# Performance work log

Measured on AMD Instinct MI355X. Metric: run time of the kernel, lower is better.

## Reference

```python
import jax, jax.numpy as jnp
import numpy as np

D_MODEL = 256
D_INNER = 512   # expand_factor * d_model
D_STATE = 64
DT_RANK = 4     # ceil(d_model / 64)
D_CONV = 4
B = 8
L = 144


def setup_inputs() -> dict:
    key = jax.random.key(0)
    ks = jax.random.split(key, 8)
    s = lambda k, shp, sc=0.02: jax.random.normal(k, shp, jnp.float32) * sc
    x = jax.random.normal(ks[0], (B, L, D_MODEL), jnp.float32)
    lastin = jnp.zeros((B, D_INNER, D_STATE), jnp.float32)  # accepted but unused by the scan
    W_in = s(ks[1], (2 * D_INNER, D_MODEL))              # in_proj (no bias)
    conv_w = s(ks[2], (D_INNER, 1, D_CONV), 0.1)          # depthwise conv kernel [O, I/groups, K]
    conv_b = jnp.zeros((D_INNER,), jnp.float32)
    W_x = s(ks[3], (DT_RANK + 2 * D_STATE, D_INNER))      # x_proj (no bias)
    W_dt = s(ks[4], (D_INNER, DT_RANK), 0.1)
    b_dt = jnp.full((D_INNER,), -4.0, jnp.float32)        # softplus -> small dt, like mamba init
    A_log = jnp.log(jnp.tile(jnp.arange(1, D_STATE + 1, dtype=jnp.float32), (D_INNER, 1)))
    Dp = jnp.ones((D_INNER,), jnp.float32)
    W_out = s(ks[5], (D_MODEL, D_INNER))                  # out_proj (no bias)
    return dict(x=x, lastin=lastin, W_in=W_in, conv_w=conv_w, conv_b=conv_b,
                W_x=W_x, W_dt=W_dt, b_dt=b_dt, A_log=A_log, Dp=Dp, W_out=W_out)


def _forward(x, lastin, W_in, conv_w, conv_b, W_x, W_dt, b_dt, A_log, Dp, W_out):
    # in_proj and split
    xz = jnp.einsum('bld,ed->ble', x, W_in)               # [B, L, 2*d_inner]
    ix, z = jnp.split(xz, 2, axis=-1)

    # depthwise causal-ish conv1d: torch padding=2 then slice [:L] == padding (2, 1)
    ix = jnp.swapaxes(ix, 1, 2)                            # [B, d_inner, L]
    ix = jax.lax.conv_general_dilated(
        ix, conv_w, window_strides=(1,), padding=[(2, 1)],
        feature_group_count=D_INNER, dimension_numbers=('NCH', 'OIH', 'NCH'))
    ix = ix + conv_b[None, :, None]
    ix = jnp.swapaxes(ix, 1, 2)                            # [B, L, d_inner]
    ix = jax.nn.silu(ix)

    # ssm parameterization
    A = -jnp.exp(A_log)                                    # [d_inner, d_state]
    dBC = jnp.einsum('bld,ed->ble', ix, W_x)               # [B, L, dt_rank + 2*d_state]
    dt_r = dBC[..., :DT_RANK]
    Bm = dBC[..., DT_RANK:DT_RANK + D_STATE]               # [B, L, d_state]
    Cm = dBC[..., DT_RANK + D_STATE:]                      # [B, L, d_state]
    delta = jax.nn.softplus(jnp.einsum('blr,dr->bld', dt_r, W_dt) + b_dt)  # [B, L, d_inner]

    # discretization
    deltaA = jnp.exp(delta[..., None] * A)                 # [B, L, d_inner, d_state]
    BX = (delta * ix)[..., None] * Bm[:, :, None, :]       # [B, L, d_inner, d_state]

    # sequential selective scan: h_t = deltaA_t * h_{t-1} + BX_t
    def step(h, inp):
        dA_t, bx_t = inp
        h = dA_t * h + bx_t
        return h, h

    h0 = jnp.zeros((x.shape[0], D_INNER, D_STATE), x.dtype)
    _, hs = jax.lax.scan(step, h0, (jnp.moveaxis(deltaA, 1, 0), jnp.moveaxis(BX, 1, 0)))
    # hs: [L, B, d_inner, d_state]

    y = jnp.einsum('lbdn,lbn->bld', hs, jnp.moveaxis(Cm, 1, 0))  # [B, L, d_inner]
    y = y + Dp * ix

    out = jnp.einsum('bld,ed->ble', y * jax.nn.silu(z), W_out)   # [B, L, d_model]
    return out


def reference(x, lastin, W_in, conv_w, conv_b, W_x, W_dt, b_dt, A_log, Dp, W_out):
    return _forward(x, lastin, W_in, conv_w, conv_b, W_x, W_dt, b_dt, A_log, Dp, W_out)
```

## Files before the change

kernel.cpp:

```cpp
#include <hip/hip_runtime.h>

#define B_SZ 8
#define L_SEQ 144
#define NTOK 1152
#define D_MODEL 256
#define D_INNER 512
#define D_STATE 64
#define DT_RANK 4
#define NDBC 132
#define SLAB 152064

typedef __attribute__((ext_vector_type(8))) short bf16x8;
typedef __attribute__((ext_vector_type(4))) float f32x4;

__device__ __forceinline__ void cvt8(const float4& f0, const float4& f1,
                                     int4& hi, int4& lo) {
    const float f[8] = {f0.x, f0.y, f0.z, f0.w, f1.x, f1.y, f1.z, f1.w};
    unsigned h[8], l[8];
#pragma unroll
    for (int e = 0; e < 8; ++e) {
        const unsigned u = __float_as_uint(f[e]);
        const unsigned t = u + 0x7FFFu + ((u >> 16) & 1u);
        h[e] = t >> 16;
        l[e] = __float_as_uint(f[e] - __uint_as_float(t & 0xFFFF0000u)) >> 16;
    }
    hi = make_int4((int)(h[0] | (h[1] << 16)), (int)(h[2] | (h[3] << 16)),
                   (int)(h[4] | (h[5] << 16)), (int)(h[6] | (h[7] << 16)));
    lo = make_int4((int)(l[0] | (l[1] << 16)), (int)(l[2] | (l[3] << 16)),
                   (int)(l[4] | (l[5] << 16)), (int)(l[6] | (l[7] << 16)));
}

__device__ __forceinline__ void unpack8(const int4& p0, const int4& p1,
                                        bf16x8& hv, bf16x8& lv) {
    const unsigned u[8] = {(unsigned)p0.x, (unsigned)p0.y, (unsigned)p0.z,
                           (unsigned)p0.w, (unsigned)p1.x, (unsigned)p1.y,
                           (unsigned)p1.z, (unsigned)p1.w};
    int h[4], l[4];
#pragma unroll
    for (int i = 0; i < 4; ++i) {
        h[i] = (int)((u[2 * i] >> 16) | (u[2 * i + 1] & 0xFFFF0000u));
        l[i] = (int)((u[2 * i] & 0xFFFFu) | (u[2 * i + 1] << 16));
    }
    hv = *(bf16x8*)h;
    lv = *(bf16x8*)l;
}

#define LW 40
__global__ __launch_bounds__(256) void gemm1_mfma(const float* __restrict__ W_in,
                                                  const float* __restrict__ x,
                                                  float* __restrict__ xz) {
    __shared__ unsigned short Ah[64][LW], Al[64][LW], Bh[64][LW], Bl[64][LW];
    const int tid = threadIdx.x;
    const int m0 = blockIdx.y * 64, n0 = blockIdx.x * 64;
    const int r = tid >> 2, kq = (tid & 3) * 8;
    const int w = tid >> 6, lane = tid & 63;
    const int wm = (w & 1) * 32, wn = (w >> 1) * 32;
    const int fr = lane & 15, fk = (lane >> 4) * 8;
    f32x4 acc[2][2] = {};
    float4 a0, a1, b0, b1;

    auto loadG = [&](const int k0) {
        const float* ap = W_in + (size_t)(m0 + r) * D_MODEL + k0 + kq;
        const float* bp = x    + (size_t)(n0 + r) * D_MODEL + k0 + kq;
        a0 = *(const float4*)ap; a1 = *(const float4*)(ap + 4);
        b0 = *(const float4*)bp; b1 = *(const float4*)(bp + 4);
    };

    loadG(0);
    for (int k0 = 0; k0 < D_MODEL; k0 += 32) {
        int4 hi, lo;
        __syncthreads();
        cvt8(a0, a1, hi, lo);
        *(int4*)&Ah[r][kq] = hi; *(int4*)&Al[r][kq] = lo;
        cvt8(b0, b1, hi, lo);
        *(int4*)&Bh[r][kq] = hi; *(int4*)&Bl[r][kq] = lo;
        __syncthreads();
        if (k0 + 32 < D_MODEL) loadG(k0 + 32);
        bf16x8 ah[2], al[2], bh[2], bl[2];
#pragma unroll
        for (int i = 0; i < 2; ++i) {
            ah[i] = *(const bf16x8*)&Ah[wm + 16 * i + fr][fk];
            al[i] = *(const bf16x8*)&Al[wm + 16 * i + fr][fk];
            bh[i] = *(const bf16x8*)&Bh[wn + 16 * i + fr][fk];
            bl[i] = *(const bf16x8*)&Bl[wn + 16 * i + fr][fk];
        }
#pragma unroll
        for (int i = 0; i < 2; ++i)
#pragma unroll
            for (int j = 0; j < 2; ++j) {
                acc[i][j] = __builtin_amdgcn_mfma_f32_16x16x32_bf16(ah[i], bh[j], acc[i][j], 0, 0, 0);
                acc[i][j] = __builtin_amdgcn_mfma_f32_16x16x32_bf16(ah[i], bl[j], acc[i][j], 0, 0, 0);
                acc[i][j] = __builtin_amdgcn_mfma_f32_16x16x32_bf16(al[i], bh[j], acc[i][j], 0, 0, 0);
            }
    }
    const int orow = (lane >> 4) * 4;
#pragma unroll
    for (int i = 0; i < 2; ++i)
#pragma unroll
        for (int j = 0; j < 2; ++j)
#pragma unroll
            for (int q = 0; q < 4; ++q)
                xz[(size_t)(m0 + wm + 16 * i + orow + q) * NTOK
                   + n0 + wn + 16 * j + fr] = acc[i][j][q];
}

__device__ __forceinline__ int bc_perm(const int p) {
    return (p < DT_RANK) ? p
         : (((p - DT_RANK) & 1) ? (DT_RANK + D_STATE + ((p - DT_RANK) >> 1))
                                : (DT_RANK + ((p - DT_RANK) >> 1)));
}

__global__ __launch_bounds__(256) void gemm2_mfma(const float* __restrict__ xz,
                                                  const float* __restrict__ W_x,
                                                  float* __restrict__ slab,
                                                  const float* __restrict__ cw,
                                                  const float* __restrict__ cb) {
    __shared__ unsigned short Ah[64][LW], Al[64][LW], Bh[64][LW], Bl[64][LW];
    const int tid = threadIdx.x;
    const int n0 = blockIdx.x * 64;
    const int m0 = blockIdx.y * 64;
    const int kbeg = blockIdx.z * 64;
    const int ar = tid >> 3, ac8 = (tid & 7) * 8;
    const int br = tid >> 2, bq8 = (tid & 3) * 8;
    const int brow = bc_perm(n0 + br);
    const int w = tid >> 6, lane = tid & 63;
    const int wm = (w & 1) * 32, wn = (w >> 1) * 32;
    const int fr = lane & 15, fk = (lane >> 4) * 8;
    const int t = (m0 + ac8) % L_SEQ;
    f32x4 acc[2][2] = {};
    slab += (size_t)blockIdx.z * SLAB;

#pragma unroll
    for (int ks = 0; ks < 2; ++ks) {
        const int k0 = kbeg + ks * 32;
        const int d = k0 + ar;
        const float* row = xz + (size_t)d * NTOK + m0 + ac8;
        const float4 a0 = *(const float4*)row;
        const float4 a1 = *(const float4*)(row + 4);
        const float xm2 = (t > 0) ? row[-2] : 0.f;
        const float xm1 = (t > 0) ? row[-1] : 0.f;
        const float xp8 = (t < L_SEQ - 8) ? row[8] : 0.f;
        const float4 cw4 = *(const float4*)(cw + d * 4);
        const float cbv = cb[d];
        float4 bv0 = make_float4(0.f, 0.f, 0.f, 0.f), bv1 = bv0;
        if (n0 + br < NDBC) {
            const float* bp = W_x + (size_t)brow * D_INNER + k0 + bq8;
            bv0 = *(const float4*)bp; bv1 = *(const float4*)(bp + 4);
        }
        __syncthreads();
        {
            const float in[11] = {xm2, xm1, a0.x, a0.y, a0.z, a0.w,
                                  a1.x, a1.y, a1.z, a1.w, xp8};
#pragma unroll
            for (int j = 0; j < 8; ++j) {
                float s = cbv;
                s = fmaf(cw4.x, in[j + 0], s);
                s = fmaf(cw4.y, in[j + 1], s);
                s = fmaf(cw4.z, in[j + 2], s);
                s = fmaf(cw4.w, in[j + 3], s);
                const float g = s * __builtin_amdgcn_rcpf(1.f + __expf(-s));
                const unsigned u = __float_as_uint(g);
                const unsigned tt = u + 0x7FFFu + ((u >> 16) & 1u);
                Ah[ac8 + j][ar] = (unsigned short)(tt >> 16);
                Al[ac8 + j][ar] = (unsigned short)(__float_as_uint(
                                     g - __uint_as_float(tt & 0xFFFF0000u)) >> 16);
            }
            int4 hi, lo;
            cvt8(bv0, bv1, hi, lo);
            *(int4*)&Bh[br][bq8] = hi; *(int4*)&Bl[br][bq8] = lo;
        }
        __syncthreads();
        bf16x8 ah[2], al[2], bh[2], bl[2];
#pragma unroll
        for (int i = 0; i < 2; ++i) {
            ah[i] = *(const bf16x8*)&Ah[wm + 16 * i + fr][fk];
            al[i] = *(const bf16x8*)&Al[wm + 16 * i + fr][fk];
            bh[i] = *(const bf16x8*)&Bh[wn + 16 * i + fr][fk];
            bl[i] = *(const bf16x8*)&Bl[wn + 16 * i + fr][fk];
        }
#pragma unroll
        for (int i = 0; i < 2; ++i)
#pragma unroll
            for (int j = 0; j < 2; ++j) {
                acc[i][j] = __builtin_amdgcn_mfma_f32_16x16x32_bf16(ah[i], bh[j], acc[i][j], 0, 0, 0);
                acc[i][j] = __builtin_amdgcn_mfma_f32_16x16x32_bf16(ah[i], bl[j], acc[i][j], 0, 0, 0);
                acc[i][j] = __builtin_amdgcn_mfma_f32_16x16x32_bf16(al[i], bh[j], acc[i][j], 0, 0, 0);
            }
    }
    const int orow = (lane >> 4) * 4;
#pragma unroll
    for (int i = 0; i < 2; ++i)
#pragma unroll
        for (int j = 0; j < 2; ++j) {
            const int gn = n0 + wn + 16 * j + fr;
            if (gn < NDBC)
#pragma unroll
                for (int q = 0; q < 4; ++q)
                    slab[(size_t)(m0 + wm + 16 * i + orow + q) * NDBC + gn]
                        = acc[i][j][q];
        }
}

__global__ __launch_bounds__(256) void gemm3_mfma(const unsigned* __restrict__ gpk,
                                                  const float* __restrict__ W_out,
                                                  float* __restrict__ slab) {
    const int tid = threadIdx.x;
    const int n0 = blockIdx.x * 64, m0 = blockIdx.y * 64;
    const int kbeg = blockIdx.z * 64;
    const int w = tid >> 6, lane = tid & 63;
    const int wm = (w & 1) * 32, wn = (w >> 1) * 32;
    const int fr = lane & 15, fk = (lane >> 4) * 8;
    f32x4 acc[2][2] = {};
    slab += (size_t)blockIdx.z * (NTOK * D_MODEL);
#pragma unroll
    for (int ks = 0; ks < 2; ++ks) {
        const int k0 = kbeg + ks * 32;
        bf16x8 ah[2], al[2], bh[2], bl[2];
#pragma unroll
        for (int i = 0; i < 2; ++i) {
            const unsigned* ap = gpk + (size_t)(m0 + wm + 16 * i + fr) * D_INNER + k0 + fk;
            unpack8(*(const int4*)ap, *(const int4*)(ap + 4), ah[i], al[i]);
        }
#pragma unroll
        for (int j = 0; j < 2; ++j) {
            const float* bp = W_out + (size_t)(n0 + wn + 16 * j + fr) * D_INNER + k0 + fk;
            int4 hi, lo;
            cvt8(*(const float4*)bp, *(const float4*)(bp + 4), hi, lo);
            bh[j] = *(bf16x8*)&hi;
            bl[j] = *(bf16x8*)&lo;
        }
#pragma unroll
        for (int i = 0; i < 2; ++i)
#pragma unroll
            for (int j = 0; j < 2; ++j) {
                acc[i][j] = __builtin_amdgcn_mfma_f32_16x16x32_bf16(ah[i], bh[j], acc[i][j], 0, 0, 0);
                acc[i][j] = __builtin_amdgcn_mfma_f32_16x16x32_bf16(ah[i], bl[j], acc[i][j], 0, 0, 0);
                acc[i][j] = __builtin_amdgcn_mfma_f32_16x16x32_bf16(al[i], bh[j], acc[i][j], 0, 0, 0);
            }
    }
    const int orow = (lane >> 4) * 4;
#pragma unroll
    for (int i = 0; i < 2; ++i)
#pragma unroll
        for (int j = 0; j < 2; ++j)
#pragma unroll
            for (int q = 0; q < 4; ++q)
                slab[(size_t)(m0 + wm + 16 * i + orow + q) * D_MODEL
                     + n0 + wn + 16 * j + fr] = acc[i][j][q];
}

__global__ __launch_bounds__(256) void reduce8_k(const float4* __restrict__ in,
                                                 float4* __restrict__ out,
                                                 const int n4, const int s4) {
    const int i = blockIdx.x * 256 + threadIdx.x;
    if (i >= n4) return;
    float4 a = in[i];
#pragma unroll
    for (int s = 1; s < 8; ++s) {
        const float4 b = in[i + s * s4];
        a.x += b.x; a.y += b.y; a.z += b.z; a.w += b.w;
    }
    out[i] = a;
}

__device__ __forceinline__ float bcast(const float v, const int i) {
    return __int_as_float(__builtin_amdgcn_readlane(__float_as_int(v), i));
}

template<int CNT>
__device__ __forceinline__ void scan_chunk(const float* __restrict__ dBC,
                                           const float* __restrict__ xz,
                                           unsigned* __restrict__ gpk,
                                           float (*__restrict__ Pw)[65],
                                           const int d, const int base, const int t0,
                                           const float An2, const float4 wdt,
                                           const float bdt, const float dpv,
                                           const float4 cw4, const float cbv,
                                           const int lane, float& h) {
    float delta_r = 0.f, dix_r = 0.f, dpix_r = 0.f, sz_r = 0.f;
    if (lane < CNT) {
        const int t = t0 + lane;
        const int tok = base + t;
        const float* row = xz + (size_t)d * NTOK + tok;
        float s0 = cbv;
        if (t >= 2) s0 = fmaf(cw4.x, row[-2], s0);
        if (t >= 1) s0 = fmaf(cw4.y, row[-1], s0);
        s0 = fmaf(cw4.z, row[0], s0);
        if (t < L_SEQ - 1) s0 = fmaf(cw4.w, row[1], s0);
        const float ixv = s0 * __builtin_amdgcn_rcpf(1.f + __expf(-s0));

        const float4 dt4 = *(const float4*)(dBC + (size_t)tok * NDBC);
        float s = fmaf(dt4.x, wdt.x, bdt);
        s = fmaf(dt4.y, wdt.y, s);
        s = fmaf(dt4.z, wdt.z, s);
        s = fmaf(dt4.w, wdt.w, s);
        const float delta = fmaxf(s, 0.f) + __logf(1.f + __expf(-fabsf(s)));
        const float zv = xz[(size_t)(D_INNER + d) * NTOK + tok];
        delta_r = delta;
        dix_r   = delta * ixv;
        dpix_r  = dpv * ixv;
        sz_r    = zv * __builtin_amdgcn_rcpf(1.f + __expf(-zv));
    }
#pragma unroll
    for (int i = 0; i < CNT; ++i) {
        const float2 bc = *(const float2*)(dBC + (size_t)(base + t0 + i) * NDBC
                                           + DT_RANK + 2 * lane);
        const float dlt = bcast(delta_r, i);
        const float dxv = bcast(dix_r, i);
        const float dA = __builtin_amdgcn_exp2f(dlt * An2);
        h = fmaf(dA, h, dxv * bc.x);
        Pw[i][lane] = h * bc.y;
    }
    const int tl = lane & 31, hf = lane >> 5;
    float s2 = 0.f;
    if (tl < CNT) {
#pragma unroll
        for (int j = 0; j < 32; ++j) s2 += Pw[tl][hf * 32 + j];
    }
    s2 += __shfl_xor(s2, 32, 64);
    if (hf == 0 && tl < CNT) {
        const float g = (s2 + dpix_r) * sz_r;
        const unsigned u = __float_as_uint(g);
        const unsigned t = u + 0x7FFFu + ((u >> 16) & 1u);
        const unsigned lo16 = __float_as_uint(
            g - __uint_as_float(t & 0xFFFF0000u)) >> 16;
        gpk[(size_t)(base + t0 + tl) * D_INNER + d] = (t & 0xFFFF0000u) | lo16;
    }
}

__global__ __launch_bounds__(256) void scan_k(const float* __restrict__ dBC,
                                              const float* __restrict__ xz,
                                              const float* __restrict__ W_dt,
                                              const float* __restrict__ b_dt,
                                              const float* __restrict__ A_log,
                                              const float* __restrict__ Dp,
                                              const float* __restrict__ conv_w,
                                              const float* __restrict__ conv_b,
                                              unsigned* __restrict__ gpk) {
    __shared__ float P[4][32][65];
    const int w = threadIdx.x >> 6, lane = threadIdx.x & 63;
    const int b = blockIdx.x >> 7, dg = blockIdx.x & 127;
    const int d = (dg << 2) | w;
    const int base = b * L_SEQ;
    const float An2 = -__expf(A_log[(d << 6) + lane]) * 1.44269504088896f;
    const float4 wdt = *(const float4*)(W_dt + (d << 2));
    const float bdt = b_dt[d], dpv = Dp[d];
    const float4 cw4 = *(const float4*)(conv_w + (d << 2));
    const float cbv = conv_b[d];
    float h = 0.f;
    scan_chunk<32>(dBC, xz, gpk, P[w], d, base, 0,   An2, wdt, bdt, dpv, cw4, cbv, lane, h);
    scan_chunk<32>(dBC, xz, gpk, P[w], d, base, 32,  An2, wdt, bdt, dpv, cw4, cbv, lane, h);
    scan_chunk<32>(dBC, xz, gpk, P[w], d, base, 64,  An2, wdt, bdt, dpv, cw4, cbv, lane, h);
    scan_chunk<32>(dBC, xz, gpk, P[w], d, base, 96,  An2, wdt, bdt, dpv, cw4, cbv, lane, h);
    scan_chunk<16>(dBC, xz, gpk, P[w], d, base, 128, An2, wdt, bdt, dpv, cw4, cbv, lane, h);
}

extern "C" void kernel_launch(void* const* d_in, const int* in_sizes, int n_in,
                              void* d_out, int out_size, void* d_ws, size_t ws_size,
                              hipStream_t stream) {
    const float* x      = (const float*)d_in[0];
    const float* W_in   = (const float*)d_in[2];
    const float* conv_w = (const float*)d_in[3];
    const float* conv_b = (const float*)d_in[4];
    const float* W_x    = (const float*)d_in[5];
    const float* W_dt   = (const float*)d_in[6];
    const float* b_dt   = (const float*)d_in[7];
    const float* A_log  = (const float*)d_in[8];
    const float* Dp     = (const float*)d_in[9];
    const float* W_out  = (const float*)d_in[10];
    float* out = (float*)d_out;

    float* ws  = (float*)d_ws;
    float* xz  = ws;
    float* dBC = xz + 1179648;
    float* sl3 = dBC + 152064;
    unsigned* gpk = (unsigned*)(sl3 + 8 * SLAB);
    float* sl6 = (float*)(gpk + NTOK * D_INNER);

    gemm1_mfma<<<dim3(18, 16), 256, 0, stream>>>(W_in, x, xz);
    gemm2_mfma<<<dim3(3, 18, 8), 256, 0, stream>>>(xz, W_x, sl3, conv_w, conv_b);
    reduce8_k<<<dim3(149), 256, 0, stream>>>((const float4*)sl3, (float4*)dBC,
                                             NTOK * NDBC / 4, NTOK * NDBC / 4);
    scan_k<<<dim3(B_SZ * 128), 256, 0, stream>>>(dBC, xz, W_dt, b_dt, A_log, Dp,
                                                 conv_w, conv_b, gpk);
    gemm3_mfma<<<dim3(4, 18, 8), 256, 0, stream>>>(gpk, W_out, sl6);
    reduce8_k<<<dim3(288), 256, 0, stream>>>((const float4*)sl6, (float4*)out,
                                             NTOK * D_MODEL / 4, NTOK * D_MODEL / 4);
}
```

Before: 130.5 us.

## Replace split-K slabs and reduce kernels with in-block warp split-K reduction

```diff
diff --git a/kernel.cpp b/kernel.cpp
--- a/kernel.cpp
+++ b/kernel.cpp
@@ -8,7 +8,6 @@
 #define D_STATE 64
 #define DT_RANK 4
 #define NDBC 132
-#define SLAB 152064
 
 typedef __attribute__((ext_vector_type(8))) short bf16x8;
 typedef __attribute__((ext_vector_type(4))) float f32x4;
@@ -43,6 +42,12 @@
     }
     hv = *(bf16x8*)h;
     lv = *(bf16x8*)l;
+}
+
+__device__ __forceinline__ int bc_perm(const int p) {
+    return (p < DT_RANK) ? p
+         : (((p - DT_RANK) & 1) ? (DT_RANK + D_STATE + ((p - DT_RANK) >> 1))
+                                : (DT_RANK + ((p - DT_RANK) >> 1)));
 }
 
 #define LW 40
@@ -104,135 +109,160 @@
                    + n0 + wn + 16 * j + fr] = acc[i][j][q];
 }
 
-__device__ __forceinline__ int bc_perm(const int p) {
-    return (p < DT_RANK) ? p
-         : (((p - DT_RANK) & 1) ? (DT_RANK + D_STATE + ((p - DT_RANK) >> 1))
-                                : (DT_RANK + ((p - DT_RANK) >> 1)));
-}
-
 __global__ __launch_bounds__(256) void gemm2_mfma(const float* __restrict__ xz,
                                                   const float* __restrict__ W_x,
-                                                  float* __restrict__ slab,
+                                                  float* __restrict__ dBC,
                                                   const float* __restrict__ cw,
                                                   const float* __restrict__ cb) {
-    __shared__ unsigned short Ah[64][LW], Al[64][LW], Bh[64][LW], Bl[64][LW];
+    __shared__ union {
+        unsigned short st[4][4][64][LW];
+        float red[4][4096];
+    } sm;
     const int tid = threadIdx.x;
     const int n0 = blockIdx.x * 64;
     const int m0 = blockIdx.y * 64;
-    const int kbeg = blockIdx.z * 64;
-    const int ar = tid >> 3, ac8 = (tid & 7) * 8;
-    const int br = tid >> 2, bq8 = (tid & 3) * 8;
-    const int brow = bc_perm(n0 + br);
     const int w = tid >> 6, lane = tid & 63;
-    const int wm = (w & 1) * 32, wn = (w >> 1) * 32;
+    const int kw = w * 128;
     const int fr = lane & 15, fk = (lane >> 4) * 8;
-    const int t = (m0 + ac8) % L_SEQ;
-    f32x4 acc[2][2] = {};
-    slab += (size_t)blockIdx.z * SLAB;
-
-#pragma unroll
-    for (int ks = 0; ks < 2; ++ks) {
-        const int k0 = kbeg + ks * 32;
-        const int d = k0 + ar;
-        const float* row = xz + (size_t)d * NTOK + m0 + ac8;
-        const float4 a0 = *(const float4*)row;
-        const float4 a1 = *(const float4*)(row + 4);
-        const float xm2 = (t > 0) ? row[-2] : 0.f;
-        const float xm1 = (t > 0) ? row[-1] : 0.f;
-        const float xp8 = (t < L_SEQ - 8) ? row[8] : 0.f;
-        const float4 cw4 = *(const float4*)(cw + d * 4);
-        const float cbv = cb[d];
-        float4 bv0 = make_float4(0.f, 0.f, 0.f, 0.f), bv1 = bv0;
-        if (n0 + br < NDBC) {
-            const float* bp = W_x + (size_t)brow * D_INNER + k0 + bq8;
-            bv0 = *(const float4*)bp; bv1 = *(const float4*)(bp + 4);
-        }
-        __syncthreads();
-        {
-            const float in[11] = {xm2, xm1, a0.x, a0.y, a0.z, a0.w,
-                                  a1.x, a1.y, a1.z, a1.w, xp8};
+    f32x4 acc[4][4] = {};
+
+    float apre[4][11];
+    float4 cwp[4];
+    float cbp[4];
+
+    auto loadA = [&](const int k0) {
+#pragma unroll
+        for (int jj = 0; jj < 4; ++jj) {
+            const int id = jj * 64 + lane;
+            const int dl = id >> 3, oct = id & 7;
+            const int d = k0 + dl;
+            const float* row = xz + (size_t)d * NTOK + m0 + oct * 8;
+            const int t = (m0 + oct * 8) % L_SEQ;
+            apre[jj][0] = (t > 0) ? row[-2] : 0.f;
+            apre[jj][1] = (t > 0) ? row[-1] : 0.f;
+            const float4 r0 = *(const float4*)row;
+            const float4 r1 = *(const float4*)(row + 4);
+            apre[jj][2] = r0.x; apre[jj][3] = r0.y; apre[jj][4] = r0.z; apre[jj][5] = r0.w;
+            apre[jj][6] = r1.x; apre[jj][7] = r1.y; apre[jj][8] = r1.z; apre[jj][9] = r1.w;
+            apre[jj][10] = (t < L_SEQ - 8) ? row[8] : 0.f;
+            cwp[jj] = *(const float4*)(cw + d * 4);
+            cbp[jj] = cb[d];
+        }
+    };
+
+    loadA(kw);
+#pragma unroll
+    for (int m = 0; m < 4; ++m) {
+        const int k0 = kw + m * 32;
+#pragma unroll
+        for (int jj = 0; jj < 4; ++jj) {
+            const int id = jj * 64 + lane;
+            const int dl = id >> 3, oct = id & 7;
 #pragma unroll
             for (int j = 0; j < 8; ++j) {
-                float s = cbv;
-                s = fmaf(cw4.x, in[j + 0], s);
-                s = fmaf(cw4.y, in[j + 1], s);
-                s = fmaf(cw4.z, in[j + 2], s);
-                s = fmaf(cw4.w, in[j + 3], s);
+                float s = cbp[jj];
+                s = fmaf(cwp[jj].x, apre[jj][j + 0], s);
+                s = fmaf(cwp[jj].y, apre[jj][j + 1], s);
+                s = fmaf(cwp[jj].z, apre[jj][j + 2], s);
+                s = fmaf(cwp[jj].w, apre[jj][j + 3], s);
                 const float g = s * __builtin_amdgcn_rcpf(1.f + __expf(-s));
                 const unsigned u = __float_as_uint(g);
                 const unsigned tt = u + 0x7FFFu + ((u >> 16) & 1u);
-                Ah[ac8 + j][ar] = (unsigned short)(tt >> 16);
-                Al[ac8 + j][ar] = (unsigned short)(__float_as_uint(
-                                     g - __uint_as_float(tt & 0xFFFF0000u)) >> 16);
+                sm.st[w][0][oct * 8 + j][dl] = (unsigned short)(tt >> 16);
+                sm.st[w][1][oct * 8 + j][dl] = (unsigned short)(__float_as_uint(
+                    g - __uint_as_float(tt & 0xFFFF0000u)) >> 16);
+            }
+        }
+#pragma unroll
+        for (int jj = 0; jj < 4; ++jj) {
+            const int id = jj * 64 + lane;
+            const int e = id >> 2, ko = (id & 3) * 8;
+            float4 b0 = make_float4(0.f, 0.f, 0.f, 0.f), b1 = b0;
+            if (n0 + e < NDBC) {
+                const float* bp = W_x + (size_t)bc_perm(n0 + e) * D_INNER + k0 + ko;
+                b0 = *(const float4*)bp; b1 = *(const float4*)(bp + 4);
             }
             int4 hi, lo;
-            cvt8(bv0, bv1, hi, lo);
-            *(int4*)&Bh[br][bq8] = hi; *(int4*)&Bl[br][bq8] = lo;
-        }
-        __syncthreads();
-        bf16x8 ah[2], al[2], bh[2], bl[2];
-#pragma unroll
-        for (int i = 0; i < 2; ++i) {
-            ah[i] = *(const bf16x8*)&Ah[wm + 16 * i + fr][fk];
-            al[i] = *(const bf16x8*)&Al[wm + 16 * i + fr][fk];
-            bh[i] = *(const bf16x8*)&Bh[wn + 16 * i + fr][fk];
-            bl[i] = *(const bf16x8*)&Bl[wn + 16 * i + fr][fk];
-        }
-#pragma unroll
-        for (int i = 0; i < 2; ++i)
-#pragma unroll
-            for (int j = 0; j < 2; ++j) {
+            cvt8(b0, b1, hi, lo);
+            *(int4*)&sm.st[w][2][e][ko] = hi;
+            *(int4*)&sm.st[w][3][e][ko] = lo;
+        }
+        if (m < 3) loadA(k0 + 32);
+        bf16x8 ah[4], al[4], bh[4], bl[4];
+#pragma unroll
+        for (int i = 0; i < 4; ++i) {
+            ah[i] = *(const bf16x8*)&sm.st[w][0][16 * i + fr][fk];
+            al[i] = *(const bf16x8*)&sm.st[w][1][16 * i + fr][fk];
+            bh[i] = *(const bf16x8*)&sm.st[w][2][16 * i + fr][fk];
+            bl[i] = *(const bf16x8*)&sm.st[w][3][16 * i + fr][fk];
+        }
+#pragma unroll
+        for (int i = 0; i < 4; ++i)
+#pragma unroll
+            for (int j = 0; j < 4; ++j) {
                 acc[i][j] = __builtin_amdgcn_mfma_f32_16x16x32_bf16(ah[i], bh[j], acc[i][j], 0, 0, 0);
                 acc[i][j] = __builtin_amdgcn_mfma_f32_16x16x32_bf16(ah[i], bl[j], acc[i][j], 0, 0, 0);
                 acc[i][j] = __builtin_amdgcn_mfma_f32_16x16x32_bf16(al[i], bh[j], acc[i][j], 0, 0, 0);
             }
     }
+    __syncthreads();
     const int orow = (lane >> 4) * 4;
 #pragma unroll
-    for (int i = 0; i < 2; ++i)
-#pragma unroll
-        for (int j = 0; j < 2; ++j) {
-            const int gn = n0 + wn + 16 * j + fr;
-            if (gn < NDBC)
-#pragma unroll
-                for (int q = 0; q < 4; ++q)
-                    slab[(size_t)(m0 + wm + 16 * i + orow + q) * NDBC + gn]
-                        = acc[i][j][q];
-        }
+    for (int i = 0; i < 4; ++i)
+#pragma unroll
+        for (int j = 0; j < 4; ++j)
+#pragma unroll
+            for (int q = 0; q < 4; ++q)
+                sm.red[w][(16 * i + orow + q) * 64 + 16 * j + fr] = acc[i][j][q];
+    __syncthreads();
+#pragma unroll
+    for (int rep = 0; rep < 4; ++rep) {
+        const int idx4 = rep * 256 + tid;
+        const int row = idx4 >> 4, col = (idx4 & 15) * 4;
+        const int gn = n0 + col;
+        if (gn < NDBC) {
+            const float4 s0 = *(const float4*)&sm.red[0][row * 64 + col];
+            const float4 s1 = *(const float4*)&sm.red[1][row * 64 + col];
+            const float4 s2 = *(const float4*)&sm.red[2][row * 64 + col];
+            const float4 s3 = *(const float4*)&sm.red[3][row * 64 + col];
+            *(float4*)(dBC + (size_t)(m0 + row) * NDBC + gn) = make_float4(
+                s0.x + s1.x + s2.x + s3.x, s0.y + s1.y + s2.y + s3.y,
+                s0.z + s1.z + s2.z + s3.z, s0.w + s1.w + s2.w + s3.w);
+        }
+    }
 }
 
 __global__ __launch_bounds__(256) void gemm3_mfma(const unsigned* __restrict__ gpk,
                                                   const float* __restrict__ W_out,
-                                                  float* __restrict__ slab) {
+                                                  float* __restrict__ out) {
+    __shared__ float red[4][4096];
     const int tid = threadIdx.x;
     const int n0 = blockIdx.x * 64, m0 = blockIdx.y * 64;
-    const int kbeg = blockIdx.z * 64;
     const int w = tid >> 6, lane = tid & 63;
-    const int wm = (w & 1) * 32, wn = (w >> 1) * 32;
+    const int kw = w * 128;
     const int fr = lane & 15, fk = (lane >> 4) * 8;
-    f32x4 acc[2][2] = {};
-    slab += (size_t)blockIdx.z * (NTOK * D_MODEL);
-#pragma unroll
-    for (int ks = 0; ks < 2; ++ks) {
-        const int k0 = kbeg + ks * 32;
-        bf16x8 ah[2], al[2], bh[2], bl[2];
-#pragma unroll
-        for (int i = 0; i < 2; ++i) {
-            const unsigned* ap = gpk + (size_t)(m0 + wm + 16 * i + fr) * D_INNER + k0 + fk;
+    f32x4 acc[4][4] = {};
+#pragma unroll
+    for (int m = 0; m < 4; ++m) {
+        const int k0 = kw + m * 32;
+        bf16x8 ah[4], al[4], bh[4], bl[4];
+#pragma unroll
+        for (int i = 0; i < 4; ++i) {
+            const unsigned* ap = gpk + (size_t)(m0 + 16 * i + fr) * D_INNER + k0 + fk;
             unpack8(*(const int4*)ap, *(const int4*)(ap + 4), ah[i], al[i]);
         }
 #pragma unroll
-        for (int j = 0; j < 2; ++j) {
-            const float* bp = W_out + (size_t)(n0 + wn + 16 * j + fr) * D_INNER + k0 + fk;
+        for (int j = 0; j < 4; ++j) {
+            const float* bp = W_out + (size_t)(n0 + 16 * j + fr) * D_INNER + k0 + fk;
             int4 hi, lo;
             cvt8(*(const float4*)bp, *(const float4*)(bp + 4), hi, lo);
             bh[j] = *(bf16x8*)&hi;
             bl[j] = *(bf16x8*)&lo;
         }
 #pragma unroll
-        for (int i = 0; i < 2; ++i)
-#pragma unroll
-            for (int j = 0; j < 2; ++j) {
+        for (int i = 0; i < 4; ++i)
+#pragma unroll
+            for (int j = 0; j < 4; ++j) {
                 acc[i][j] = __builtin_amdgcn_mfma_f32_16x16x32_bf16(ah[i], bh[j], acc[i][j], 0, 0, 0);
                 acc[i][j] = __builtin_amdgcn_mfma_f32_16x16x32_bf16(ah[i], bl[j], acc[i][j], 0, 0, 0);
                 acc[i][j] = __builtin_amdgcn_mfma_f32_16x16x32_bf16(al[i], bh[j], acc[i][j], 0, 0, 0);
@@ -240,27 +270,25 @@
     }
     const int orow = (lane >> 4) * 4;
 #pragma unroll
-    for (int i = 0; i < 2; ++i)
-#pragma unroll
-        for (int j = 0; j < 2; ++j)
+    for (int i = 0; i < 4; ++i)
+#pragma unroll
+        for (int j = 0; j < 4; ++j)
 #pragma unroll
             for (int q = 0; q < 4; ++q)
-                slab[(size_t)(m0 + wm + 16 * i + orow + q) * D_MODEL
-                     + n0 + wn + 16 * j + fr] = acc[i][j][q];
-}
-
-__global__ __launch_bounds__(256) void reduce8_k(const float4* __restrict__ in,
-                                                 float4* __restrict__ out,
-                                                 const int n4, const int s4) {
-    const int i = blockIdx.x * 256 + threadIdx.x;
-    if (i >= n4) return;
-    float4 a = in[i];
-#pragma unroll
-    for (int s = 1; s < 8; ++s) {
-        const float4 b = in[i + s * s4];
-        a.x += b.x; a.y += b.y; a.z += b.z; a.w += b.w;
-    }
-    out[i] = a;
+                red[w][(16 * i + orow + q) * 64 + 16 * j + fr] = acc[i][j][q];
+    __syncthreads();
+#pragma unroll
+    for (int rep = 0; rep < 4; ++rep) {
+        const int idx4 = rep * 256 + tid;
+        const int row = idx4 >> 4, col = (idx4 & 15) * 4;
+        const float4 s0 = *(const float4*)&red[0][row * 64 + col];
+        const float4 s1 = *(const float4*)&red[1][row * 64 + col];
+        const float4 s2 = *(const float4*)&red[2][row * 64 + col];
+        const float4 s3 = *(const float4*)&red[3][row * 64 + col];
+        *(float4*)(out + (size_t)(m0 + row) * D_MODEL + n0 + col) = make_float4(
+            s0.x + s1.x + s2.x + s3.x, s0.y + s1.y + s2.y + s3.y,
+            s0.z + s1.z + s2.z + s3.z, s0.w + s1.w + s2.w + s3.w);
+    }
 }
 
 __device__ __forceinline__ float bcast(const float v, const int i) {
@@ -373,17 +401,11 @@
     float* ws  = (float*)d_ws;
     float* xz  = ws;
     float* dBC = xz + 1179648;
-    float* sl3 = dBC + 152064;
-    unsigned* gpk = (unsigned*)(sl3 + 8 * SLAB);
-    float* sl6 = (float*)(gpk + NTOK * D_INNER);
+    unsigned* gpk = (unsigned*)(dBC + 152064);
 
     gemm1_mfma<<<dim3(18, 16), 256, 0, stream>>>(W_in, x, xz);
-    gemm2_mfma<<<dim3(3, 18, 8), 256, 0, stream>>>(xz, W_x, sl3, conv_w, conv_b);
-    reduce8_k<<<dim3(149), 256, 0, stream>>>((const float4*)sl3, (float4*)dBC,
-                                             NTOK * NDBC / 4, NTOK * NDBC / 4);
+    gemm2_mfma<<<dim3(3, 18), 256, 0, stream>>>(xz, W_x, dBC, conv_w, conv_b);
     scan_k<<<dim3(B_SZ * 128), 256, 0, stream>>>(dBC, xz, W_dt, b_dt, A_log, Dp,
                                                  conv_w, conv_b, gpk);
-    gemm3_mfma<<<dim3(4, 18, 8), 256, 0, stream>>>(gpk, W_out, sl6);
-    reduce8_k<<<dim3(288), 256, 0, stream>>>((const float4*)sl6, (float4*)out,
-                                             NTOK * D_MODEL / 4, NTOK * D_MODEL / 4);
-}
+    gemm3_mfma<<<dim3(4, 18), 256, 0, stream>>>(gpk, W_out, out);
+}
```

Result: slower. 143.7 us (+10.1%).

## Fuse out_proj split-K reduction into gemm3 via in-block LDS reduce

Applied to the files above, without the earlier changes.

```diff
diff --git a/kernel.cpp b/kernel.cpp
--- a/kernel.cpp
+++ b/kernel.cpp
@@ -43,6 +43,12 @@
     }
     hv = *(bf16x8*)h;
     lv = *(bf16x8*)l;
+}
+
+__device__ __forceinline__ int bc_perm(const int p) {
+    return (p < DT_RANK) ? p
+         : (((p - DT_RANK) & 1) ? (DT_RANK + D_STATE + ((p - DT_RANK) >> 1))
+                                : (DT_RANK + ((p - DT_RANK) >> 1)));
 }
 
 #define LW 40
@@ -102,12 +108,6 @@
             for (int q = 0; q < 4; ++q)
                 xz[(size_t)(m0 + wm + 16 * i + orow + q) * NTOK
                    + n0 + wn + 16 * j + fr] = acc[i][j][q];
-}
-
-__device__ __forceinline__ int bc_perm(const int p) {
-    return (p < DT_RANK) ? p
-         : (((p - DT_RANK) & 1) ? (DT_RANK + D_STATE + ((p - DT_RANK) >> 1))
-                                : (DT_RANK + ((p - DT_RANK) >> 1)));
 }
 
 __global__ __launch_bounds__(256) void gemm2_mfma(const float* __restrict__ xz,
@@ -203,50 +203,50 @@
 
 __global__ __launch_bounds__(256) void gemm3_mfma(const unsigned* __restrict__ gpk,
                                                   const float* __restrict__ W_out,
-                                                  float* __restrict__ slab) {
+                                                  float* __restrict__ out) {
+    __shared__ float red[4][16][64];
     const int tid = threadIdx.x;
-    const int n0 = blockIdx.x * 64, m0 = blockIdx.y * 64;
-    const int kbeg = blockIdx.z * 64;
+    const int n0 = blockIdx.x * 64, m0 = blockIdx.y * 16;
     const int w = tid >> 6, lane = tid & 63;
-    const int wm = (w & 1) * 32, wn = (w >> 1) * 32;
+    const int kw = w * 128;
     const int fr = lane & 15, fk = (lane >> 4) * 8;
-    f32x4 acc[2][2] = {};
-    slab += (size_t)blockIdx.z * (NTOK * D_MODEL);
-#pragma unroll
-    for (int ks = 0; ks < 2; ++ks) {
-        const int k0 = kbeg + ks * 32;
-        bf16x8 ah[2], al[2], bh[2], bl[2];
-#pragma unroll
-        for (int i = 0; i < 2; ++i) {
-            const unsigned* ap = gpk + (size_t)(m0 + wm + 16 * i + fr) * D_INNER + k0 + fk;
-            unpack8(*(const int4*)ap, *(const int4*)(ap + 4), ah[i], al[i]);
-        }
-#pragma unroll
-        for (int j = 0; j < 2; ++j) {
-            const float* bp = W_out + (size_t)(n0 + wn + 16 * j + fr) * D_INNER + k0 + fk;
+    f32x4 acc[4] = {};
+#pragma unroll
+    for (int m = 0; m < 4; ++m) {
+        const int k0 = kw + m * 32;
+        bf16x8 ah, al, bh[4], bl[4];
+        const unsigned* ap = gpk + (size_t)(m0 + fr) * D_INNER + k0 + fk;
+        unpack8(*(const int4*)ap, *(const int4*)(ap + 4), ah, al);
+#pragma unroll
+        for (int j = 0; j < 4; ++j) {
+            const float* bp = W_out + (size_t)(n0 + 16 * j + fr) * D_INNER + k0 + fk;
             int4 hi, lo;
             cvt8(*(const float4*)bp, *(const float4*)(bp + 4), hi, lo);
             bh[j] = *(bf16x8*)&hi;
             bl[j] = *(bf16x8*)&lo;
         }
 #pragma unroll
-        for (int i = 0; i < 2; ++i)
-#pragma unroll
-            for (int j = 0; j < 2; ++j) {
-                acc[i][j] = __builtin_amdgcn_mfma_f32_16x16x32_bf16(ah[i], bh[j], acc[i][j], 0, 0, 0);
-                acc[i][j] = __builtin_amdgcn_mfma_f32_16x16x32_bf16(ah[i], bl[j], acc[i][j], 0, 0, 0);
-                acc[i][j] = __builtin_amdgcn_mfma_f32_16x16x32_bf16(al[i], bh[j], acc[i][j], 0, 0, 0);
-            }
+        for (int j = 0; j < 4; ++j) {
+            acc[j] = __builtin_amdgcn_mfma_f32_16x16x32_bf16(ah, bh[j], acc[j], 0, 0, 0);
+            acc[j] = __builtin_amdgcn_mfma_f32_16x16x32_bf16(ah, bl[j], acc[j], 0, 0, 0);
+            acc[j] = __builtin_amdgcn_mfma_f32_16x16x32_bf16(al, bh[j], acc[j], 0, 0, 0);
+        }
     }
     const int orow = (lane >> 4) * 4;
 #pragma unroll
-    for (int i = 0; i < 2; ++i)
-#pragma unroll
-        for (int j = 0; j < 2; ++j)
-#pragma unroll
-            for (int q = 0; q < 4; ++q)
-                slab[(size_t)(m0 + wm + 16 * i + orow + q) * D_MODEL
-                     + n0 + wn + 16 * j + fr] = acc[i][j][q];
+    for (int j = 0; j < 4; ++j)
+#pragma unroll
+        for (int q = 0; q < 4; ++q)
+            red[w][orow + q][16 * j + fr] = acc[j][q];
+    __syncthreads();
+    const int row = tid >> 4, col = (tid & 15) * 4;
+    const float4 s0 = *(const float4*)&red[0][row][col];
+    const float4 s1 = *(const float4*)&red[1][row][col];
+    const float4 s2 = *(const float4*)&red[2][row][col];
+    const float4 s3 = *(const float4*)&red[3][row][col];
+    *(float4*)(out + (size_t)(m0 + row) * D_MODEL + n0 + col) = make_float4(
+        s0.x + s1.x + s2.x + s3.x, s0.y + s1.y + s2.y + s3.y,
+        s0.z + s1.z + s2.z + s3.z, s0.w + s1.w + s2.w + s3.w);
 }
 
 __global__ __launch_bounds__(256) void reduce8_k(const float4* __restrict__ in,
@@ -375,7 +375,6 @@
     float* dBC = xz + 1179648;
     float* sl3 = dBC + 152064;
     unsigned* gpk = (unsigned*)(sl3 + 8 * SLAB);
-    float* sl6 = (float*)(gpk + NTOK * D_INNER);
 
     gemm1_mfma<<<dim3(18, 16), 256, 0, stream>>>(W_in, x, xz);
     gemm2_mfma<<<dim3(3, 18, 8), 256, 0, stream>>>(xz, W_x, sl3, conv_w, conv_b);
@@ -383,7 +382,5 @@
                                              NTOK * NDBC / 4, NTOK * NDBC / 4);
     scan_k<<<dim3(B_SZ * 128), 256, 0, stream>>>(dBC, xz, W_dt, b_dt, A_log, Dp,
                                                  conv_w, conv_b, gpk);
-    gemm3_mfma<<<dim3(4, 18, 8), 256, 0, stream>>>(gpk, W_out, sl6);
-    reduce8_k<<<dim3(288), 256, 0, stream>>>((const float4*)sl6, (float4*)out,
-                                             NTOK * D_MODEL / 4, NTOK * D_MODEL / 4);
-}
+    gemm3_mfma<<<dim3(4, 72), 256, 0, stream>>>(gpk, W_out, out);
+}
```

Result: no change. 129.9 us, median of 2 (-0.5%).
